# Optimization experiments

Measured on AMD Instinct MI355X. Metric: run time of the kernel, lower is better.

## Reference

```python
import jax, jax.numpy as jnp
import numpy as np

HIDDEN = 512
NUM_HEADS = 8


def setup_inputs() -> dict:
    key = jax.random.key(0)
    ks = jax.random.split(key, 8)
    Tq, Tk, Cq, Ck, H = 1, 65536, 512, 512, HIDDEN
    s = 1.0 / np.sqrt(H)
    return {
        "Q": jax.random.normal(ks[0], (Tq, Cq), jnp.float32),
        "K": jax.random.normal(ks[1], (Tk, Ck), jnp.float32),
        "Wq": jax.random.normal(ks[2], (H, Cq), jnp.float32) * s,
        "bq": jax.random.normal(ks[3], (H,), jnp.float32) * s,
        "Wk": jax.random.normal(ks[4], (H, Ck), jnp.float32) * s,
        "bk": jax.random.normal(ks[5], (H,), jnp.float32) * s,
        "Wout": jax.random.normal(ks[6], (1, NUM_HEADS), jnp.float32) * 0.3,
        "bout": jax.random.normal(ks[7], (1,), jnp.float32) * 0.3,
    }


def reference(Q, K, Wq, bq, Wk, bk, Wout, bout):
    h = NUM_HEADS
    H = Wq.shape[0]
    d = H // h  # per-head dim
    # linear + ReLU projections
    Ql = jax.nn.relu(Q @ Wq.T + bq)          # [1, H]
    Kl = jax.nn.relu(K @ Wk.T + bk)          # [Tk, H]
    # split into heads (T_q == 1 is required by linear_out)
    Qh = Ql.reshape(h, d)                    # [h, d]
    Kh = Kl.reshape(-1, h, d)                # [Tk, h, d]
    # per-head scores, scaled by sqrt(d_head); dropout rate 0 -> identity
    scores = jnp.einsum('hd,thd->th', Qh, Kh) / (d ** 0.5)  # [Tk, h]
    # learned per-head fusion, then softmax over the T_k axis
    logits = scores @ Wout.T + bout          # [Tk, 1]
    return jax.nn.softmax(logits, axis=0)    # [Tk, 1]
```

## Files before the change

### kernel.cpp

```cpp
#include <hip/hip_runtime.h>
#include <hip/hip_fp16.h>

#define CDIM 512
#define ROWS 65536

typedef _Float16 half8  __attribute__((ext_vector_type(8)));
typedef __fp16   fp16x2 __attribute__((ext_vector_type(2)));
typedef float    f32x16 __attribute__((ext_vector_type(16)));

#define GLD_LDS16(gp, lp) __builtin_amdgcn_global_load_lds( \
    (const __attribute__((address_space(1))) unsigned int*)(gp), \
    (__attribute__((address_space(3))) unsigned int*)(lp), 16, 0, 0)

__device__ __forceinline__ half8 cvt8(float4 f0, float4 f1) {
    union { fp16x2 h2[4]; half8 h8; } u;
    u.h2[0] = __builtin_amdgcn_cvt_pkrtz(f0.x, f0.y);
    u.h2[1] = __builtin_amdgcn_cvt_pkrtz(f0.z, f0.w);
    u.h2[2] = __builtin_amdgcn_cvt_pkrtz(f1.x, f1.y);
    u.h2[3] = __builtin_amdgcn_cvt_pkrtz(f1.z, f1.w);
    return u.h8;
}

__global__ void prep_kernel(const float* __restrict__ Q, const float* __restrict__ Wq,
                            const float* __restrict__ bq, const float* __restrict__ Wout,
                            const float* __restrict__ Wk,
                            float* __restrict__ v, _Float16* __restrict__ Wkf) {
    __shared__ float qs[CDIM];
    const int t = threadIdx.x;
    if (blockIdx.x < 32) {
        qs[t] = Q[t]; qs[t + 256] = Q[t + 256];
        __syncthreads();
        const int jj  = t >> 4;
        const int sub = t & 15;
        const int j   = blockIdx.x * 16 + jj;
        const float4* w4 = (const float4*)(Wq + (size_t)j * CDIM + sub * 32);
        const float4* q4 = (const float4*)(qs + sub * 32);
        float s = 0.f;
        #pragma unroll
        for (int i = 0; i < 8; ++i) {
            float4 w = w4[i]; float4 q = q4[i];
            s = fmaf(w.x, q.x, s); s = fmaf(w.y, q.y, s);
            s = fmaf(w.z, q.z, s); s = fmaf(w.w, q.w, s);
        }
        s += __shfl_xor(s, 1); s += __shfl_xor(s, 2);
        s += __shfl_xor(s, 4); s += __shfl_xor(s, 8);
        if (sub == 0) {
            s += bq[j];
            s = fmaxf(s, 0.f);
            v[j] = s * Wout[j >> 6] * 0.125f;
        }
    } else {
        const int gid = (blockIdx.x - 32) * 256 + t;
        const int jb  = gid >> 11;
        const int kc  = (gid >> 6) & 31;
        const int l   = gid & 63;
        const int j   = jb * 32 + (l & 31);
        const int k   = kc * 16 + (l >> 5) * 8;
        const float* src = Wk + (size_t)j * CDIM + k;
        float4 f0 = *(const float4*)(src);
        float4 f1 = *(const float4*)(src + 4);
        *(half8*)(Wkf + (size_t)gid * 8) = cvt8(f0, f1);
    }
}

__global__ __launch_bounds__(512, 1) void score_kernel(
    const float* __restrict__ Kmat, const _Float16* __restrict__ Wkf,
    const float* __restrict__ bk, const float* __restrict__ v,
    float* __restrict__ logits)
{
    __shared__ alignas(16) char Bb[2][65536];

    const int tid  = threadIdx.x;
    const int lane = tid & 63;
    const int wave = tid >> 6;
    const int l31  = lane & 31;
    const int lhi  = lane >> 5;
    const int rowbase = blockIdx.x * 256;

    #pragma unroll
    for (int i = 0; i < 8; ++i)
        GLD_LDS16((const char*)Wkf + i * 8192 + tid * 16, Bb[0] + i * 8192 + tid * 16);

    half8 a[32];
    {
        const float* ab = Kmat + (size_t)(rowbase + wave * 32 + l31) * CDIM + lhi * 8;
        #pragma unroll
        for (int kc = 0; kc < 32; ++kc) {
            float4 f0 = *(const float4*)(ab + kc * 16);
            float4 f1 = *(const float4*)(ab + kc * 16 + 4);
            a[kc] = cvt8(f0, f1);
        }
    }

    float part[16];
    #pragma unroll
    for (int r = 0; r < 16; ++r) part[r] = 0.f;

    __syncthreads();

    for (int c = 0; c < 8; ++c) {
        const int cur = c & 1;

        if (c < 7) {
            const char* src = (const char*)Wkf + (size_t)(c + 1) * 65536;
            #pragma unroll
            for (int i = 0; i < 8; ++i)
                GLD_LDS16(src + i * 8192 + tid * 16, Bb[cur ^ 1] + i * 8192 + tid * 16);
        }

        const int jg0 = c * 64 + l31;
        const float bj0 = bk[jg0],      vj0 = v[jg0];
        const float bj1 = bk[jg0 + 32], vj1 = v[jg0 + 32];

        f32x16 acc0, acc1;
        #pragma unroll
        for (int r = 0; r < 16; ++r) { acc0[r] = 0.f; acc1[r] = 0.f; }

        #pragma unroll
        for (int kc = 0; kc < 32; ++kc) {
            half8 b0 = *(const half8*)(Bb[cur] + kc * 1024 + lane * 16);
            half8 b1 = *(const half8*)(Bb[cur] + (32 + kc) * 1024 + lane * 16);
            acc0 = __builtin_amdgcn_mfma_f32_32x32x16_f16(a[kc], b0, acc0, 0, 0, 0);
            acc1 = __builtin_amdgcn_mfma_f32_32x32x16_f16(a[kc], b1, acc1, 0, 0, 0);
        }

        #pragma unroll
        for (int r = 0; r < 16; ++r)
            part[r] += fmaxf(acc0[r] + bj0, 0.f) * vj0 + fmaxf(acc1[r] + bj1, 0.f) * vj1;

        __syncthreads();
    }

    {
        float q0[8];
        #pragma unroll
        for (int i = 0; i < 8; ++i) {
            const bool b = lane & 1;
            float keep = b ? part[i + 8] : part[i];
            float send = b ? part[i] : part[i + 8];
            q0[i] = keep + __shfl_xor(send, 1);
        }
        float q1[4];
        #pragma unroll
        for (int i = 0; i < 4; ++i) {
            const bool b = lane & 2;
            float keep = b ? q0[i + 4] : q0[i];
            float send = b ? q0[i] : q0[i + 4];
            q1[i] = keep + __shfl_xor(send, 2);
        }
        float q2[2];
        #pragma unroll
        for (int i = 0; i < 2; ++i) {
            const bool b = lane & 4;
            float keep = b ? q1[i + 2] : q1[i];
            float send = b ? q1[i] : q1[i + 2];
            q2[i] = keep + __shfl_xor(send, 4);
        }
        float q3;
        {
            const bool b = lane & 8;
            float keep = b ? q2[1] : q2[0];
            float send = b ? q2[0] : q2[1];
            q3 = keep + __shfl_xor(send, 8);
        }
        float s = q3 + __shfl_xor(q3, 16);
        if (l31 < 16) {
            const int rr  = ((l31 & 1) << 3) | ((l31 & 2) << 1) | ((l31 & 4) >> 1) | ((l31 & 8) >> 3);
            const int row = (rr & 3) + 8 * (rr >> 2) + 4 * lhi;
            logits[rowbase + wave * 32 + row] = s;
        }
    }
}

__global__ void expsum_kernel(const float* __restrict__ logits, float* __restrict__ blocksum) {
    __shared__ float red[256];
    const int t = threadIdx.x;
    red[t] = expf(logits[blockIdx.x * 256 + t]);
    __syncthreads();
    for (int s = 128; s > 0; s >>= 1) {
        if (t < s) red[t] += red[t + s];
        __syncthreads();
    }
    if (t == 0) blocksum[blockIdx.x] = red[0];
}

__global__ void norm_kernel(const float* __restrict__ logits, const float* __restrict__ blocksum,
                            float* __restrict__ out) {
    __shared__ float red[256];
    const int t = threadIdx.x;
    red[t] = blocksum[t];
    __syncthreads();
    for (int s = 128; s > 0; s >>= 1) {
        if (t < s) red[t] += red[t + s];
        __syncthreads();
    }
    const float zinv = 1.0f / red[0];
    const int i = blockIdx.x * 256 + t;
    out[i] = expf(logits[i]) * zinv;
}

extern "C" void kernel_launch(void* const* d_in, const int* in_sizes, int n_in,
                              void* d_out, int out_size, void* d_ws, size_t ws_size,
                              hipStream_t stream) {
    const float* Q    = (const float*)d_in[0];
    const float* Kmat = (const float*)d_in[1];
    const float* Wq   = (const float*)d_in[2];
    const float* bq   = (const float*)d_in[3];
    const float* Wk   = (const float*)d_in[4];
    const float* bk   = (const float*)d_in[5];
    const float* Wout = (const float*)d_in[6];
    float* out = (float*)d_out;

    char* ws = (char*)d_ws;
    _Float16* Wkf   = (_Float16*)(ws);
    float* v        = (float*)(ws + 524288);
    float* logits   = (float*)(ws + 526336);
    float* blocksum = (float*)(ws + 788480);

    hipLaunchKernelGGL(prep_kernel,   dim3(160),  dim3(256), 0, stream, Q, Wq, bq, Wout, Wk, v, Wkf);
    hipLaunchKernelGGL(score_kernel,  dim3(256),  dim3(512), 0, stream, Kmat, Wkf, bk, v, logits);
    hipLaunchKernelGGL(expsum_kernel, dim3(256),  dim3(256), 0, stream, logits, blocksum);
    hipLaunchKernelGGL(norm_kernel,   dim3(256),  dim3(256), 0, stream, logits, blocksum, out);
}
```

Measured before the change: 62.43 us.

## Give each wave 64 rows with 4 MFMA accumulators and overlap A loads with first chunk

The score kernel now runs 256 threads per block, and each wave handles 64 K rows instead of 32. Each B fragment read from LDS is reused across two A tiles, which halves LDS traffic per MFMA. The fp32 K loads and their fp16 conversion are moved inside the first chunk's compute loop, interleaved in groups of four, so global load latency overlaps with the MFMAs. The cost is doubled register pressure (64 half8 A registers plus four accumulators), which risks spilling, and half as many waves per CU to hide latency.

```diff
diff --git a/kernel.cpp b/kernel.cpp
--- a/kernel.cpp
+++ b/kernel.cpp
@@ -63,7 +63,7 @@
     }
 }
 
-__global__ __launch_bounds__(512, 1) void score_kernel(
+__global__ __launch_bounds__(256, 1) void score_kernel(
     const float* __restrict__ Kmat, const _Float16* __restrict__ Wkf,
     const float* __restrict__ bk, const float* __restrict__ v,
     float* __restrict__ logits)
@@ -78,23 +78,16 @@
     const int rowbase = blockIdx.x * 256;
 
     #pragma unroll
-    for (int i = 0; i < 8; ++i)
-        GLD_LDS16((const char*)Wkf + i * 8192 + tid * 16, Bb[0] + i * 8192 + tid * 16);
-
-    half8 a[32];
-    {
-        const float* ab = Kmat + (size_t)(rowbase + wave * 32 + l31) * CDIM + lhi * 8;
-        #pragma unroll
-        for (int kc = 0; kc < 32; ++kc) {
-            float4 f0 = *(const float4*)(ab + kc * 16);
-            float4 f1 = *(const float4*)(ab + kc * 16 + 4);
-            a[kc] = cvt8(f0, f1);
-        }
-    }
-
-    float part[16];
+    for (int i = 0; i < 16; ++i)
+        GLD_LDS16((const char*)Wkf + i * 4096 + tid * 16, Bb[0] + i * 4096 + tid * 16);
+
+    const float* ab0 = Kmat + (size_t)(rowbase + wave * 64 + l31) * CDIM + lhi * 8;
+    const float* ab1 = ab0 + 32 * CDIM;
+
+    half8 a0[32], a1[32];
+    float part0[16], part1[16];
     #pragma unroll
-    for (int r = 0; r < 16; ++r) part[r] = 0.f;
+    for (int r = 0; r < 16; ++r) { part0[r] = 0.f; part1[r] = 0.f; }
 
     __syncthreads();
 
@@ -104,40 +97,75 @@
         if (c < 7) {
             const char* src = (const char*)Wkf + (size_t)(c + 1) * 65536;
             #pragma unroll
-            for (int i = 0; i < 8; ++i)
-                GLD_LDS16(src + i * 8192 + tid * 16, Bb[cur ^ 1] + i * 8192 + tid * 16);
-        }
-
-        const int jg0 = c * 64 + l31;
-        const float bj0 = bk[jg0],      vj0 = v[jg0];
-        const float bj1 = bk[jg0 + 32], vj1 = v[jg0 + 32];
-
-        f32x16 acc0, acc1;
-        #pragma unroll
-        for (int r = 0; r < 16; ++r) { acc0[r] = 0.f; acc1[r] = 0.f; }
-
-        #pragma unroll
-        for (int kc = 0; kc < 32; ++kc) {
-            half8 b0 = *(const half8*)(Bb[cur] + kc * 1024 + lane * 16);
-            half8 b1 = *(const half8*)(Bb[cur] + (32 + kc) * 1024 + lane * 16);
-            acc0 = __builtin_amdgcn_mfma_f32_32x32x16_f16(a[kc], b0, acc0, 0, 0, 0);
-            acc1 = __builtin_amdgcn_mfma_f32_32x32x16_f16(a[kc], b1, acc1, 0, 0, 0);
-        }
-
-        #pragma unroll
-        for (int r = 0; r < 16; ++r)
-            part[r] += fmaxf(acc0[r] + bj0, 0.f) * vj0 + fmaxf(acc1[r] + bj1, 0.f) * vj1;
-
-        __syncthreads();
-    }
-
-    {
+            for (int i = 0; i < 16; ++i)
+                GLD_LDS16(src + i * 4096 + tid * 16, Bb[cur ^ 1] + i * 4096 + tid * 16);
+        }
+
+        const int jg = c * 64 + l31;
+        const float bj0 = bk[jg],      vj0 = v[jg];
+        const float bj1 = bk[jg + 32], vj1 = v[jg + 32];
+
+        f32x16 acc00, acc01, acc10, acc11;
+        #pragma unroll
+        for (int r = 0; r < 16; ++r) { acc00[r]=0.f; acc01[r]=0.f; acc10[r]=0.f; acc11[r]=0.f; }
+
+        if (c == 0) {
+            #pragma unroll
+            for (int q = 0; q < 8; ++q) {
+                #pragma unroll
+                for (int i = 0; i < 4; ++i) {
+                    const int kc = q * 4 + i;
+                    float4 f00 = *(const float4*)(ab0 + kc * 16);
+                    float4 f01 = *(const float4*)(ab0 + kc * 16 + 4);
+                    float4 f10 = *(const float4*)(ab1 + kc * 16);
+                    float4 f11 = *(const float4*)(ab1 + kc * 16 + 4);
+                    a0[kc] = cvt8(f00, f01);
+                    a1[kc] = cvt8(f10, f11);
+                }
+                #pragma unroll
+                for (int i = 0; i < 4; ++i) {
+                    const int kc = q * 4 + i;
+                    half8 b0 = *(const half8*)(Bb[0] + kc * 1024 + lane * 16);
+                    half8 b1 = *(const half8*)(Bb[0] + (32 + kc) * 1024 + lane * 16);
+                    acc00 = __builtin_amdgcn_mfma_f32_32x32x16_f16(a0[kc], b0, acc00, 0, 0, 0);
+                    acc01 = __builtin_amdgcn_mfma_f32_32x32x16_f16(a0[kc], b1, acc01, 0, 0, 0);
+                    acc10 = __builtin_amdgcn_mfma_f32_32x32x16_f16(a1[kc], b0, acc10, 0, 0, 0);
+                    acc11 = __builtin_amdgcn_mfma_f32_32x32x16_f16(a1[kc], b1, acc11, 0, 0, 0);
+                }
+            }
+        } else {
+            #pragma unroll
+            for (int kc = 0; kc < 32; ++kc) {
+                half8 b0 = *(const half8*)(Bb[cur] + kc * 1024 + lane * 16);
+                half8 b1 = *(const half8*)(Bb[cur] + (32 + kc) * 1024 + lane * 16);
+                acc00 = __builtin_amdgcn_mfma_f32_32x32x16_f16(a0[kc], b0, acc00, 0, 0, 0);
+                acc01 = __builtin_amdgcn_mfma_f32_32x32x16_f16(a0[kc], b1, acc01, 0, 0, 0);
+                acc10 = __builtin_amdgcn_mfma_f32_32x32x16_f16(a1[kc], b0, acc10, 0, 0, 0);
+                acc11 = __builtin_amdgcn_mfma_f32_32x32x16_f16(a1[kc], b1, acc11, 0, 0, 0);
+            }
+        }
+
+        #pragma unroll
+        for (int r = 0; r < 16; ++r) {
+            part0[r] += fmaxf(acc00[r] + bj0, 0.f) * vj0 + fmaxf(acc01[r] + bj1, 0.f) * vj1;
+            part1[r] += fmaxf(acc10[r] + bj0, 0.f) * vj0 + fmaxf(acc11[r] + bj1, 0.f) * vj1;
+        }
+
+        __syncthreads();
+    }
+
+    #pragma unroll
+    for (int g = 0; g < 2; ++g) {
+        float x[16];
+        #pragma unroll
+        for (int r = 0; r < 16; ++r) x[r] = (g == 0) ? part0[r] : part1[r];
+
         float q0[8];
         #pragma unroll
         for (int i = 0; i < 8; ++i) {
             const bool b = lane & 1;
-            float keep = b ? part[i + 8] : part[i];
-            float send = b ? part[i] : part[i + 8];
+            float keep = b ? x[i + 8] : x[i];
+            float send = b ? x[i] : x[i + 8];
             q0[i] = keep + __shfl_xor(send, 1);
         }
         float q1[4];
@@ -167,7 +195,7 @@
         if (l31 < 16) {
             const int rr  = ((l31 & 1) << 3) | ((l31 & 2) << 1) | ((l31 & 4) >> 1) | ((l31 & 8) >> 3);
             const int row = (rr & 3) + 8 * (rr >> 2) + 4 * lhi;
-            logits[rowbase + wave * 32 + row] = s;
+            logits[rowbase + wave * 64 + g * 32 + row] = s;
         }
     }
 }
@@ -218,7 +246,7 @@
     float* blocksum = (float*)(ws + 788480);
 
     hipLaunchKernelGGL(prep_kernel,   dim3(160),  dim3(256), 0, stream, Q, Wq, bq, Wout, Wk, v, Wkf);
-    hipLaunchKernelGGL(score_kernel,  dim3(256),  dim3(512), 0, stream, Kmat, Wkf, bk, v, logits);
+    hipLaunchKernelGGL(score_kernel,  dim3(256),  dim3(256), 0, stream, Kmat, Wkf, bk, v, logits);
     hipLaunchKernelGGL(expsum_kernel, dim3(256),  dim3(256), 0, stream, logits, blocksum);
     hipLaunchKernelGGL(norm_kernel,   dim3(256),  dim3(256), 0, stream, logits, blocksum, out);
 }
```

After: 68.20 us. +9.2%, slower.
